# Performance work log

Measured on AMD Instinct MI355X. Metric: run time of the kernel, lower is better.

The kernel has to match this reference:

```python
import jax, jax.numpy as jnp
import numpy as np

NUM_GRAPHS = 64
BN_EPS = 1e-5


def setup_inputs() -> dict:
    key = jax.random.key(0)
    ks = jax.random.split(key, 20)
    N, E, D, H, C, L = 100_000, 1_600_000, 128, 128, 16, 4
    x = jax.random.normal(ks[0], (N, D), jnp.float32)
    edge_index = jax.random.randint(ks[1], (2, E), 0, N, jnp.int32)
    batch = jnp.sort(jax.random.randint(ks[2], (N,), 0, NUM_GRAPHS, jnp.int32))
    s = 0.05
    conv_W = jax.random.normal(ks[3], (L, D, H), jnp.float32) * s
    conv_b = jnp.zeros((L, H), jnp.float32)
    bn_gamma = jnp.ones((L, H), jnp.float32)
    bn_beta = jnp.zeros((L, H), jnp.float32)
    bn_mean = jax.random.normal(ks[4], (L, H), jnp.float32) * 0.01
    bn_var = jnp.ones((L, H), jnp.float32)
    cls_W1 = jax.random.normal(ks[5], (H, H), jnp.float32) * s
    cls_b1 = jnp.zeros((H,), jnp.float32)
    cls_W2 = jax.random.normal(ks[6], (H, C), jnp.float32) * s
    cls_b2 = jnp.zeros((C,), jnp.float32)
    nov_W1 = jax.random.normal(ks[7], (H, H), jnp.float32) * s
    nov_b1 = jnp.zeros((H,), jnp.float32)
    nov_W2 = jax.random.normal(ks[8], (H, 1), jnp.float32) * s
    nov_b2 = jnp.zeros((1,), jnp.float32)
    return {
        'x': x, 'edge_index': edge_index, 'batch': batch,
        'conv_W': conv_W, 'conv_b': conv_b,
        'bn_gamma': bn_gamma, 'bn_beta': bn_beta, 'bn_mean': bn_mean, 'bn_var': bn_var,
        'cls_W1': cls_W1, 'cls_b1': cls_b1, 'cls_W2': cls_W2, 'cls_b2': cls_b2,
        'nov_W1': nov_W1, 'nov_b1': nov_b1, 'nov_W2': nov_W2, 'nov_b2': nov_b2,
    }


def reference(x, edge_index, batch, conv_W, conv_b, bn_gamma, bn_beta, bn_mean, bn_var,
              cls_W1, cls_b1, cls_W2, cls_b2, nov_W1, nov_b1, nov_W2, nov_b2):
    N = x.shape[0]
    src, dst = edge_index[0], edge_index[1]
    # symmetric GCN normalization with self-loops: deg = in-degree + 1
    deg = jax.ops.segment_sum(jnp.ones(src.shape[0], x.dtype), dst, num_segments=N) + 1.0
    dis = jax.lax.rsqrt(deg)  # [N]
    edge_norm = (dis[src] * dis[dst])[:, None]  # [E,1]
    self_norm = (dis * dis)[:, None]            # [N,1]

    h = x
    for l in range(conv_W.shape[0]):
        hw = h @ conv_W[l]                                   # [N,H]
        agg = jax.ops.segment_sum(hw[src] * edge_norm, dst, num_segments=N)
        hw = agg + hw * self_norm + conv_b[l]                # GCNConv output
        # BatchNorm1d, eval mode (running stats); dropout is identity in eval
        hw = (hw - bn_mean[l]) * (bn_gamma[l] / jnp.sqrt(bn_var[l] + BN_EPS)) + bn_beta[l]
        h = jax.nn.relu(hw)

    pooled = jax.ops.segment_sum(h, batch, num_segments=NUM_GRAPHS)  # global_add_pool [G,H]
    logits = jax.nn.relu(pooled @ cls_W1 + cls_b1) @ cls_W2 + cls_b2           # [G,C]
    novelty = jax.nn.sigmoid(jax.nn.relu(pooled @ nov_W1 + nov_b1) @ nov_W2 + nov_b2)  # [G,1]
    return (logits, novelty)
```

## Files before the change

### kernel.cpp

```cpp
#include <hip/hip_runtime.h>
#include <hip/hip_fp16.h>
#include <cstdint>
#include <cstddef>

#define NUM_GRAPHS 64
#define HDIM 128
#define NBLK_S 256

typedef __attribute__((ext_vector_type(8))) _Float16 half8v;
typedef __attribute__((ext_vector_type(4))) float float4v;

__global__ __launch_bounds__(256) void count_hist_kernel(const int* __restrict__ dst,
                                                         int* __restrict__ cnt,
                                                         int* __restrict__ hist,
                                                         int E, int chunk, int shift, int NB) {
    __shared__ int lh[256];
    int t = threadIdx.x;
    int b = blockIdx.x;
    lh[t] = 0;
    __syncthreads();
    int beg = b * chunk;
    int end = beg + chunk; if (end > E) end = E;
    for (int i = beg + t; i < end; i += 256) {
        int d = dst[i];
        atomicAdd(&cnt[d], 1);
        atomicAdd(&lh[d >> shift], 1);
    }
    __syncthreads();
    for (int k = t; k < NB; k += 256) hist[k * NBLK_S + b] = lh[k];
}

__global__ __launch_bounds__(256) void scan_partial_kernel(const int* __restrict__ in,
                                                           int* __restrict__ blockSums, int M) {
    __shared__ int s[256];
    int t = threadIdx.x;
    int base = blockIdx.x * 4096 + t * 16;
    int local = 0;
#pragma unroll
    for (int i = 0; i < 16; ++i) {
        int idx = base + i;
        if (idx < M) local += in[idx];
    }
    s[t] = local;
    __syncthreads();
    for (int off = 128; off > 0; off >>= 1) {
        if (t < off) s[t] += s[t + off];
        __syncthreads();
    }
    if (t == 0) blockSums[blockIdx.x] = s[0];
}

__global__ __launch_bounds__(1024) void scan_blocksums_kernel(int* __restrict__ blockSums,
                                                              int* __restrict__ row_ptr_or_null,
                                                              int nb, int E, int N) {
    __shared__ int s[1024];
    int t = threadIdx.x;
    int v = (t < nb) ? blockSums[t] : 0;
    s[t] = v;
    __syncthreads();
    for (int off = 1; off < 1024; off <<= 1) {
        int u = (t >= off) ? s[t - off] : 0;
        __syncthreads();
        s[t] += u;
        __syncthreads();
    }
    if (t < nb) blockSums[t] = s[t] - v;
    if (t == 0 && row_ptr_or_null) row_ptr_or_null[N] = E;
}

__global__ __launch_bounds__(256) void scan_apply_kernel(const int* __restrict__ cnt,
                                                         const int* __restrict__ blockSums,
                                                         int* __restrict__ row_ptr,
                                                         int* __restrict__ fill,
                                                         float* __restrict__ dis, int N) {
    __shared__ int s[256];
    int t = threadIdx.x;
    int base = blockIdx.x * 4096 + t * 16;
    int c[16];
    int local = 0;
#pragma unroll
    for (int i = 0; i < 16; ++i) {
        int idx = base + i;
        c[i] = (idx < N) ? cnt[idx] : 0;
        local += c[i];
    }
    s[t] = local;
    __syncthreads();
    for (int off = 1; off < 256; off <<= 1) {
        int u = (t >= off) ? s[t - off] : 0;
        __syncthreads();
        s[t] += u;
        __syncthreads();
    }
    int pos = blockSums[blockIdx.x] + s[t] - local;
#pragma unroll
    for (int i = 0; i < 16; ++i) {
        int idx = base + i;
        if (idx < N) {
            row_ptr[idx] = pos;
            fill[idx] = pos;
            dis[idx] = rsqrtf((float)c[i] + 1.0f);
            pos += c[i];
        }
    }
}

__global__ __launch_bounds__(256) void scan_apply_generic(int* __restrict__ io,
                                                          const int* __restrict__ blockSums, int M) {
    __shared__ int s[256];
    int t = threadIdx.x;
    int base = blockIdx.x * 4096 + t * 16;
    int c[16];
    int local = 0;
#pragma unroll
    for (int i = 0; i < 16; ++i) {
        int idx = base + i;
        c[i] = (idx < M) ? io[idx] : 0;
        local += c[i];
    }
    s[t] = local;
    __syncthreads();
    for (int off = 1; off < 256; off <<= 1) {
        int u = (t >= off) ? s[t - off] : 0;
        __syncthreads();
        s[t] += u;
        __syncthreads();
    }
    int pos = blockSums[blockIdx.x] + s[t] - local;
#pragma unroll
    for (int i = 0; i < 16; ++i) {
        int idx = base + i;
        if (idx < M) {
            io[idx] = pos;
            pos += c[i];
        }
    }
}

__global__ __launch_bounds__(256) void scatter_bucket_kernel(const int* __restrict__ src,
                                                             const int* __restrict__ dst,
                                                             const int* __restrict__ hist,
                                                             int2* __restrict__ pairs,
                                                             int E, int chunk, int shift, int NB) {
    __shared__ int base[256];
    int t = threadIdx.x;
    int b = blockIdx.x;
    for (int k = t; k < NB; k += 256) base[k] = hist[k * NBLK_S + b];
    __syncthreads();
    int beg = b * chunk;
    int end = beg + chunk; if (end > E) end = E;
    for (int i = beg + t; i < end; i += 256) {
        int d = dst[i];
        int s = src[i];
        int pos = atomicAdd(&base[d >> shift], 1);
        pairs[pos] = make_int2(s, d);
    }
}

__global__ __launch_bounds__(256) void fill_pairs_kernel(const int2* __restrict__ pairs,
                                                         int* __restrict__ fill,
                                                         int* __restrict__ sorted_src, int E) {
    int i = blockIdx.x * 256 + threadIdx.x;
    if (i < E) {
        int2 p = pairs[i];
        int pos = atomicAdd(&fill[p.y], 1);
        sorted_src[pos] = p.x;
    }
}

__global__ __launch_bounds__(256) void fold_kernel(const float* __restrict__ gamma,
                                                   const float* __restrict__ beta,
                                                   const float* __restrict__ mean,
                                                   const float* __restrict__ var,
                                                   const float* __restrict__ convb,
                                                   float* __restrict__ scale,
                                                   float* __restrict__ bias, int LH) {
    int i = blockIdx.x * 256 + threadIdx.x;
    if (i < LH) {
        float gs = gamma[i] * rsqrtf(var[i] + 1e-5f);
        scale[i] = gs;
        bias[i] = (convb[i] - mean[i]) * gs + beta[i];
    }
}

__global__ __launch_bounds__(64) void pack_W_kernel(const float* __restrict__ W,
                                                    __half* __restrict__ hi,
                                                    __half* __restrict__ lo) {
    int b = blockIdx.x;
    int l = b >> 5;
    int ntile = (b >> 2) & 7;
    int kchunk = b & 3;
    int lane = threadIdx.x;
    int n = ntile * 16 + (lane & 15);
    int kbase = kchunk * 32 + (lane >> 4) * 8;
    size_t ob = ((size_t)b * 64 + lane) * 8;
#pragma unroll
    for (int j = 0; j < 8; ++j) {
        float w = W[(size_t)l * 16384 + (size_t)(kbase + j) * 128 + n];
        __half hb = __float2half_rn(w);
        float rem = w - __half2float(hb);
        hi[ob + j] = hb;
        lo[ob + j] = __float2half_rn(rem);
    }
}

__global__ __launch_bounds__(256) void gemm_mfma_f16(const __half* __restrict__ h16,
                                                     const float* __restrict__ h32,
                                                     const __half* __restrict__ Whi,
                                                     const __half* __restrict__ Wlo,
                                                     const float* __restrict__ dis,
                                                     __half* __restrict__ out, int N) {
    int wave = threadIdx.x >> 6;
    int lane = threadIdx.x & 63;
    int lrow = lane & 15;
    int lk8 = lane >> 4;
    int mbase = blockIdx.x * 128 + wave * 32;

    float4v acc[2][8];
#pragma unroll
    for (int mt = 0; mt < 2; ++mt)
#pragma unroll
        for (int nt = 0; nt < 8; ++nt) {
            acc[mt][nt][0] = 0.f; acc[mt][nt][1] = 0.f;
            acc[mt][nt][2] = 0.f; acc[mt][nt][3] = 0.f;
        }

    const half8v* BH = (const half8v*)Whi;
    const half8v* BL = (const half8v*)Wlo;
    const half8v* H8 = (const half8v*)h16;

    for (int kc = 0; kc < 4; ++kc) {
        half8v a[2];
#pragma unroll
        for (int mt = 0; mt < 2; ++mt) {
            int node = mbase + mt * 16 + lrow;
            if (node < N) {
                if (h32) {
                    const float4* hp = (const float4*)&h32[(size_t)node * HDIM + kc * 32 + lk8 * 8];
                    float4 f0 = hp[0], f1 = hp[1];
                    a[mt][0] = (_Float16)f0.x; a[mt][1] = (_Float16)f0.y;
                    a[mt][2] = (_Float16)f0.z; a[mt][3] = (_Float16)f0.w;
                    a[mt][4] = (_Float16)f1.x; a[mt][5] = (_Float16)f1.y;
                    a[mt][6] = (_Float16)f1.z; a[mt][7] = (_Float16)f1.w;
                } else {
                    a[mt] = H8[(size_t)node * 16 + kc * 4 + lk8];
                }
            } else {
#pragma unroll
                for (int j = 0; j < 8; ++j) a[mt][j] = (_Float16)0;
            }
        }
#pragma unroll
        for (int nt = 0; nt < 8; ++nt) {
            half8v bh = BH[(size_t)(nt * 4 + kc) * 64 + lane];
            half8v bl = BL[(size_t)(nt * 4 + kc) * 64 + lane];
#pragma unroll
            for (int mt = 0; mt < 2; ++mt) {
                acc[mt][nt] = __builtin_amdgcn_mfma_f32_16x16x32_f16(a[mt], bh, acc[mt][nt], 0, 0, 0);
                acc[mt][nt] = __builtin_amdgcn_mfma_f32_16x16x32_f16(a[mt], bl, acc[mt][nt], 0, 0, 0);
            }
        }
    }

#pragma unroll
    for (int mt = 0; mt < 2; ++mt) {
#pragma unroll
        for (int r = 0; r < 4; ++r) {
            int node = mbase + mt * 16 + lk8 * 4 + r;
            if (node < N) {
                float dn = dis[node];
#pragma unroll
                for (int nt = 0; nt < 8; ++nt)
                    out[(size_t)node * HDIM + nt * 16 + lrow] = __float2half_rn(acc[mt][nt][r] * dn);
            }
        }
    }
}

__device__ inline void acc_add8(float4& a, uint2 v) {
    float2 f0 = __half22float2(*(__half2*)&v.x);
    float2 f1 = __half22float2(*(__half2*)&v.y);
    a.x += f0.x; a.y += f0.y; a.z += f1.x; a.w += f1.y;
}

__global__ __launch_bounds__(256) void agg_kernel(const __half* __restrict__ hwp,
                                                  const int* __restrict__ row_ptr,
                                                  const int* __restrict__ ss,
                                                  const float* __restrict__ dis,
                                                  const float* __restrict__ scale,
                                                  const float* __restrict__ bias,
                                                  __half* __restrict__ hout, int N) {
    int wave = threadIdx.x >> 6;
    int lane = threadIdx.x & 63;
    int n = blockIdx.x * 4 + wave;
    if (n >= N) return;
    int hid = lane >> 5;
    int l32 = lane & 31;
    const uint2* rows = (const uint2*)hwp;

    float4 acc0 = make_float4(0.f, 0.f, 0.f, 0.f);
    float4 acc1 = make_float4(0.f, 0.f, 0.f, 0.f);

    if (hid == 0) {
        uint2 sv = rows[(size_t)n * 32 + l32];
        acc_add8(acc0, sv);
    }

    int e0 = row_ptr[n];
    int e1 = row_ptr[n + 1];
    int e = e0;

    for (; e + 15 < e1; e += 16) {
        int sA = ss[e + 0],  sB = ss[e + 1],  sC = ss[e + 2],  sD = ss[e + 3];
        int sE = ss[e + 4],  sF = ss[e + 5],  sG = ss[e + 6],  sH = ss[e + 7];
        int sI = ss[e + 8],  sJ = ss[e + 9],  sK = ss[e + 10], sL = ss[e + 11];
        int sM = ss[e + 12], sN = ss[e + 13], sO = ss[e + 14], sP = ss[e + 15];
        int q0 = hid ? sB : sA;
        int q1 = hid ? sD : sC;
        int q2 = hid ? sF : sE;
        int q3 = hid ? sH : sG;
        int q4 = hid ? sJ : sI;
        int q5 = hid ? sL : sK;
        int q6 = hid ? sN : sM;
        int q7 = hid ? sP : sO;
        uint2 v0 = rows[(size_t)q0 * 32 + l32];
        uint2 v1 = rows[(size_t)q1 * 32 + l32];
        uint2 v2 = rows[(size_t)q2 * 32 + l32];
        uint2 v3 = rows[(size_t)q3 * 32 + l32];
        uint2 v4 = rows[(size_t)q4 * 32 + l32];
        uint2 v5 = rows[(size_t)q5 * 32 + l32];
        uint2 v6 = rows[(size_t)q6 * 32 + l32];
        uint2 v7 = rows[(size_t)q7 * 32 + l32];
        acc_add8(acc0, v0);
        acc_add8(acc1, v1);
        acc_add8(acc0, v2);
        acc_add8(acc1, v3);
        acc_add8(acc0, v4);
        acc_add8(acc1, v5);
        acc_add8(acc0, v6);
        acc_add8(acc1, v7);
    }
    for (; e + 7 < e1; e += 8) {
        int sA = ss[e + 0], sB = ss[e + 1], sC = ss[e + 2], sD = ss[e + 3];
        int sE = ss[e + 4], sF = ss[e + 5], sG = ss[e + 6], sH = ss[e + 7];
        int q0 = hid ? sB : sA;
        int q1 = hid ? sD : sC;
        int q2 = hid ? sF : sE;
        int q3 = hid ? sH : sG;
        uint2 v0 = rows[(size_t)q0 * 32 + l32];
        uint2 v1 = rows[(size_t)q1 * 32 + l32];
        uint2 v2 = rows[(size_t)q2 * 32 + l32];
        uint2 v3 = rows[(size_t)q3 * 32 + l32];
        acc_add8(acc0, v0);
        acc_add8(acc1, v1);
        acc_add8(acc0, v2);
        acc_add8(acc1, v3);
    }
    for (; e + 1 < e1; e += 2) {
        int sA = ss[e], sB = ss[e + 1];
        int q0 = hid ? sB : sA;
        uint2 v0 = rows[(size_t)q0 * 32 + l32];
        acc_add8(acc0, v0);
    }
    if (e < e1) {
        if (hid == 0) {
            int sA = ss[e];
            uint2 v0 = rows[(size_t)sA * 32 + l32];
            acc_add8(acc1, v0);
        }
    }
    acc0.x += acc1.x; acc0.y += acc1.y; acc0.z += acc1.z; acc0.w += acc1.w;

    acc0.x += __shfl_xor(acc0.x, 32);
    acc0.y += __shfl_xor(acc0.y, 32);
    acc0.z += __shfl_xor(acc0.z, 32);
    acc0.w += __shfl_xor(acc0.w, 32);

    if (hid == 0) {
        float dn = dis[n];
        int f0 = l32 * 4;
        float4 sc = *(const float4*)&scale[f0];
        float4 bs = *(const float4*)&bias[f0];
        float y0 = fmaxf(dn * acc0.x * sc.x + bs.x, 0.f);
        float y1 = fmaxf(dn * acc0.y * sc.y + bs.y, 0.f);
        float y2 = fmaxf(dn * acc0.z * sc.z + bs.z, 0.f);
        float y3 = fmaxf(dn * acc0.w * sc.w + bs.w, 0.f);
        __half2 o0 = __floats2half2_rn(y0, y1);
        __half2 o1 = __floats2half2_rn(y2, y3);
        uint2 ov;
        ov.x = *(unsigned*)&o0;
        ov.y = *(unsigned*)&o1;
        ((uint2*)hout)[(size_t)n * 32 + l32] = ov;
    }
}

__global__ __launch_bounds__(256) void pool_kernel(const __half* __restrict__ h,
                                                   const int* __restrict__ batch,
                                                   float* __restrict__ pooled, int N) {
    int t = threadIdx.x;
    int grp = t >> 6;
    int lane = t & 63;
    int n0 = blockIdx.x * 64 + grp * 16;
    if (n0 >= N) return;
    int nend = n0 + 16; if (nend > N) nend = N;
    const __half2* h2 = (const __half2*)h;

    float2 acc = make_float2(0.f, 0.f);
    int cur = batch[n0];
    for (int n = n0; n < nend; ++n) {
        int gn = batch[n];
        if (gn != cur) {
            atomicAdd(&pooled[cur * HDIM + lane * 2], acc.x);
            atomicAdd(&pooled[cur * HDIM + lane * 2 + 1], acc.y);
            acc = make_float2(0.f, 0.f);
            cur = gn;
        }
        float2 v = __half22float2(h2[(size_t)n * 64 + lane]);
        acc.x += v.x;
        acc.y += v.y;
    }
    atomicAdd(&pooled[cur * HDIM + lane * 2], acc.x);
    atomicAdd(&pooled[cur * HDIM + lane * 2 + 1], acc.y);
}

__global__ __launch_bounds__(128) void head_kernel(const float* __restrict__ pooled,
                                                   const float* __restrict__ cW1, const float* __restrict__ cb1,
                                                   const float* __restrict__ cW2, const float* __restrict__ cb2,
                                                   const float* __restrict__ nW1, const float* __restrict__ nb1,
                                                   const float* __restrict__ nW2, const float* __restrict__ nb2,
                                                   float* __restrict__ out) {
    __shared__ float p[128];
    __shared__ float hid[128];
    int g = blockIdx.x, t = threadIdx.x;
    p[t] = pooled[g * HDIM + t];
    __syncthreads();

    float a = cb1[t];
    for (int k = 0; k < 128; ++k) a += p[k] * cW1[k * 128 + t];
    hid[t] = fmaxf(a, 0.f);
    __syncthreads();
    if (t < 16) {
        float acc = cb2[t];
        for (int j = 0; j < 128; ++j) acc += hid[j] * cW2[j * 16 + t];
        out[g * 16 + t] = acc;
    }
    __syncthreads();

    float b = nb1[t];
    for (int k = 0; k < 128; ++k) b += p[k] * nW1[k * 128 + t];
    hid[t] = fmaxf(b, 0.f);
    __syncthreads();
    if (t == 0) {
        float acc = nb2[0];
        for (int j = 0; j < 128; ++j) acc += hid[j] * nW2[j];
        out[NUM_GRAPHS * 16 + g] = 1.f / (1.f + expf(-acc));
    }
}

extern "C" void kernel_launch(void* const* d_in, const int* in_sizes, int n_in,
                              void* d_out, int out_size, void* d_ws, size_t ws_size,
                              hipStream_t stream) {
    const float* x       = (const float*)d_in[0];
    const int*   ei      = (const int*)d_in[1];
    const int*   batch   = (const int*)d_in[2];
    const float* conv_W  = (const float*)d_in[3];
    const float* conv_b  = (const float*)d_in[4];
    const float* bn_g    = (const float*)d_in[5];
    const float* bn_b    = (const float*)d_in[6];
    const float* bn_m    = (const float*)d_in[7];
    const float* bn_v    = (const float*)d_in[8];
    const float* cW1     = (const float*)d_in[9];
    const float* cb1     = (const float*)d_in[10];
    const float* cW2     = (const float*)d_in[11];
    const float* cb2     = (const float*)d_in[12];
    const float* nW1     = (const float*)d_in[13];
    const float* nb1     = (const float*)d_in[14];
    const float* nW2     = (const float*)d_in[15];
    const float* nb2     = (const float*)d_in[16];

    const int N = in_sizes[2];
    const int E = in_sizes[1] / 2;
    const int L = in_sizes[3] / (128 * 128);
    const int H = HDIM;

    const int* src = ei;
    const int* dst = ei + E;

    int shift = 9;
    while ((((N - 1) >> shift) + 1) > 256) ++shift;
    const int NB = ((N - 1) >> shift) + 1;
    const int M = NB * NBLK_S;
    const int chunk = (E + NBLK_S - 1) / NBLK_S;

    char* w = (char*)d_ws;
    size_t o = 0;
    auto alloc = [&](size_t bytes) -> void* {
        void* p = w + o;
        o = (o + bytes + 255) & ~(size_t)255;
        return p;
    };
    int nscanN = (N + 4095) / 4096;
    int nscanM = (M + 4095) / 4096;
    int nscanMax = nscanN > nscanM ? nscanN : nscanM;

    int*    cnt        = (int*)alloc((size_t)N * 4);
    int*    fill       = (int*)alloc((size_t)N * 4);
    int*    row_ptr    = (int*)alloc((size_t)(N + 1) * 4);
    float*  dis        = (float*)alloc((size_t)N * 4);
    float*  scale      = (float*)alloc((size_t)L * H * 4);
    float*  bias       = (float*)alloc((size_t)L * H * 4);
    int*    blockSums  = (int*)alloc((size_t)nscanMax * 4);
    int*    hist       = (int*)alloc((size_t)M * 4);
    int2*   pairs      = (int2*)alloc((size_t)E * 8);
    int*    sorted_src = (int*)alloc((size_t)E * 4);
    __half* Whi        = (__half*)alloc((size_t)L * H * H * 2);
    __half* Wlo        = (__half*)alloc((size_t)L * H * H * 2);
    __half* bufA       = (__half*)alloc((size_t)N * H * 2);
    __half* bufB       = (__half*)alloc((size_t)N * H * 2);
    float*  pooled     = (float*)alloc((size_t)NUM_GRAPHS * H * 4);

    hipMemsetAsync(cnt, 0, (size_t)N * 4, stream);
    hipMemsetAsync(pooled, 0, (size_t)NUM_GRAPHS * H * 4, stream);

    count_hist_kernel<<<NBLK_S, 256, 0, stream>>>(dst, cnt, hist, E, chunk, shift, NB);
    scan_partial_kernel<<<nscanN, 256, 0, stream>>>(cnt, blockSums, N);
    scan_blocksums_kernel<<<1, 1024, 0, stream>>>(blockSums, row_ptr, nscanN, E, N);
    scan_apply_kernel<<<nscanN, 256, 0, stream>>>(cnt, blockSums, row_ptr, fill, dis, N);
    scan_partial_kernel<<<nscanM, 256, 0, stream>>>(hist, blockSums, M);
    scan_blocksums_kernel<<<1, 1024, 0, stream>>>(blockSums, nullptr, nscanM, 0, 0);
    scan_apply_generic<<<nscanM, 256, 0, stream>>>(hist, blockSums, M);
    scatter_bucket_kernel<<<NBLK_S, 256, 0, stream>>>(src, dst, hist, pairs, E, chunk, shift, NB);
    fill_pairs_kernel<<<(E + 255) / 256, 256, 0, stream>>>(pairs, fill, sorted_src, E);

    fold_kernel<<<(L * H + 255) / 256, 256, 0, stream>>>(bn_g, bn_b, bn_m, bn_v, conv_b,
                                                         scale, bias, L * H);
    pack_W_kernel<<<L * 32, 64, 0, stream>>>(conv_W, Whi, Wlo);

    const __half* hin = nullptr;
    for (int l = 0; l < L; ++l) {
        gemm_mfma_f16<<<(N + 127) / 128, 256, 0, stream>>>(hin, l == 0 ? x : nullptr,
                                                           Whi + (size_t)l * H * H,
                                                           Wlo + (size_t)l * H * H,
                                                           dis, bufA, N);
        agg_kernel<<<(N + 3) / 4, 256, 0, stream>>>(bufA, row_ptr, sorted_src, dis,
                                                    scale + l * H, bias + l * H, bufB, N);
        hin = bufB;
    }

    pool_kernel<<<(N + 63) / 64, 256, 0, stream>>>(bufB, batch, pooled, N);
    head_kernel<<<NUM_GRAPHS, 128, 0, stream>>>(pooled, cW1, cb1, cW2, cb2,
                                                nW1, nb1, nW2, nb2, (float*)d_out);
}
```

Before: 695.8 us.

## Split GEMM output columns across waves and keep W fragments in registers

Reorganizes the per-layer feature GEMM so each wave owns two 16-column output tiles and holds its hi/lo weight fragments in registers for the whole block. The block now covers 64 rows instead of 128, with all four waves sharing the same rows, and the grid is doubled. This drops the 64 accumulators per wave and the repeated weight reloads. In exchange, every wave reloads the same A rows, so input reads per block grow about fourfold, mostly served from cache.

```diff
diff --git a/kernel.cpp b/kernel.cpp
--- a/kernel.cpp
+++ b/kernel.cpp
@@ -204,6 +204,30 @@
     }
 }
 
+__device__ inline half8v load_a(const half8v* __restrict__ H8,
+                                const float* __restrict__ h32,
+                                int node, int kc, int lk8, int N) {
+    half8v a;
+    if (node < N) {
+        if (h32) {
+            const float4* hp = (const float4*)&h32[(size_t)node * HDIM + kc * 32 + lk8 * 8];
+            float4 f0 = hp[0], f1 = hp[1];
+            a[0] = (_Float16)f0.x; a[1] = (_Float16)f0.y;
+            a[2] = (_Float16)f0.z; a[3] = (_Float16)f0.w;
+            a[4] = (_Float16)f1.x; a[5] = (_Float16)f1.y;
+            a[6] = (_Float16)f1.z; a[7] = (_Float16)f1.w;
+        } else {
+            a = H8[(size_t)node * 16 + kc * 4 + lk8];
+        }
+    } else {
+#pragma unroll
+        for (int j = 0; j < 8; ++j) a[j] = (_Float16)0;
+    }
+    return a;
+}
+
+#define MFMA16(A, B, C) __builtin_amdgcn_mfma_f32_16x16x32_f16((A), (B), (C), 0, 0, 0)
+
 __global__ __launch_bounds__(256) void gemm_mfma_f16(const __half* __restrict__ h16,
                                                      const float* __restrict__ h32,
                                                      const __half* __restrict__ Whi,
@@ -214,64 +238,59 @@
     int lane = threadIdx.x & 63;
     int lrow = lane & 15;
     int lk8 = lane >> 4;
-    int mbase = blockIdx.x * 128 + wave * 32;
-
-    float4v acc[2][8];
-#pragma unroll
-    for (int mt = 0; mt < 2; ++mt)
-#pragma unroll
-        for (int nt = 0; nt < 8; ++nt) {
-            acc[mt][nt][0] = 0.f; acc[mt][nt][1] = 0.f;
-            acc[mt][nt][2] = 0.f; acc[mt][nt][3] = 0.f;
-        }
+    int nt0 = wave * 2;
+    int mbase = blockIdx.x * 64;
+    if (mbase >= N) return;
 
     const half8v* BH = (const half8v*)Whi;
     const half8v* BL = (const half8v*)Wlo;
     const half8v* H8 = (const half8v*)h16;
 
-    for (int kc = 0; kc < 4; ++kc) {
-        half8v a[2];
-#pragma unroll
-        for (int mt = 0; mt < 2; ++mt) {
-            int node = mbase + mt * 16 + lrow;
-            if (node < N) {
-                if (h32) {
-                    const float4* hp = (const float4*)&h32[(size_t)node * HDIM + kc * 32 + lk8 * 8];
-                    float4 f0 = hp[0], f1 = hp[1];
-                    a[mt][0] = (_Float16)f0.x; a[mt][1] = (_Float16)f0.y;
-                    a[mt][2] = (_Float16)f0.z; a[mt][3] = (_Float16)f0.w;
-                    a[mt][4] = (_Float16)f1.x; a[mt][5] = (_Float16)f1.y;
-                    a[mt][6] = (_Float16)f1.z; a[mt][7] = (_Float16)f1.w;
-                } else {
-                    a[mt] = H8[(size_t)node * 16 + kc * 4 + lk8];
-                }
-            } else {
-#pragma unroll
-                for (int j = 0; j < 8; ++j) a[mt][j] = (_Float16)0;
-            }
-        }
-#pragma unroll
-        for (int nt = 0; nt < 8; ++nt) {
-            half8v bh = BH[(size_t)(nt * 4 + kc) * 64 + lane];
-            half8v bl = BL[(size_t)(nt * 4 + kc) * 64 + lane];
-#pragma unroll
-            for (int mt = 0; mt < 2; ++mt) {
-                acc[mt][nt] = __builtin_amdgcn_mfma_f32_16x16x32_f16(a[mt], bh, acc[mt][nt], 0, 0, 0);
-                acc[mt][nt] = __builtin_amdgcn_mfma_f32_16x16x32_f16(a[mt], bl, acc[mt][nt], 0, 0, 0);
-            }
-        }
-    }
-
-#pragma unroll
-    for (int mt = 0; mt < 2; ++mt) {
+    half8v bh00 = BH[(size_t)(nt0 * 4 + 0) * 64 + lane];
+    half8v bh01 = BH[(size_t)(nt0 * 4 + 1) * 64 + lane];
+    half8v bh02 = BH[(size_t)(nt0 * 4 + 2) * 64 + lane];
+    half8v bh03 = BH[(size_t)(nt0 * 4 + 3) * 64 + lane];
+    half8v bl00 = BL[(size_t)(nt0 * 4 + 0) * 64 + lane];
+    half8v bl01 = BL[(size_t)(nt0 * 4 + 1) * 64 + lane];
+    half8v bl02 = BL[(size_t)(nt0 * 4 + 2) * 64 + lane];
+    half8v bl03 = BL[(size_t)(nt0 * 4 + 3) * 64 + lane];
+    half8v bh10 = BH[(size_t)((nt0 + 1) * 4 + 0) * 64 + lane];
+    half8v bh11 = BH[(size_t)((nt0 + 1) * 4 + 1) * 64 + lane];
+    half8v bh12 = BH[(size_t)((nt0 + 1) * 4 + 2) * 64 + lane];
+    half8v bh13 = BH[(size_t)((nt0 + 1) * 4 + 3) * 64 + lane];
+    half8v bl10 = BL[(size_t)((nt0 + 1) * 4 + 0) * 64 + lane];
+    half8v bl11 = BL[(size_t)((nt0 + 1) * 4 + 1) * 64 + lane];
+    half8v bl12 = BL[(size_t)((nt0 + 1) * 4 + 2) * 64 + lane];
+    half8v bl13 = BL[(size_t)((nt0 + 1) * 4 + 3) * 64 + lane];
+
+#pragma unroll
+    for (int mt = 0; mt < 4; ++mt) {
+        int m0 = mbase + mt * 16;
+        if (m0 >= N) break;
+        int arow = m0 + lrow;
+        half8v a0 = load_a(H8, h32, arow, 0, lk8, N);
+        half8v a1 = load_a(H8, h32, arow, 1, lk8, N);
+        half8v a2 = load_a(H8, h32, arow, 2, lk8, N);
+        half8v a3 = load_a(H8, h32, arow, 3, lk8, N);
+
+        float4v c0 = {0.f, 0.f, 0.f, 0.f};
+        float4v c1 = {0.f, 0.f, 0.f, 0.f};
+        c0 = MFMA16(a0, bh00, c0); c0 = MFMA16(a0, bl00, c0);
+        c0 = MFMA16(a1, bh01, c0); c0 = MFMA16(a1, bl01, c0);
+        c0 = MFMA16(a2, bh02, c0); c0 = MFMA16(a2, bl02, c0);
+        c0 = MFMA16(a3, bh03, c0); c0 = MFMA16(a3, bl03, c0);
+        c1 = MFMA16(a0, bh10, c1); c1 = MFMA16(a0, bl10, c1);
+        c1 = MFMA16(a1, bh11, c1); c1 = MFMA16(a1, bl11, c1);
+        c1 = MFMA16(a2, bh12, c1); c1 = MFMA16(a2, bl12, c1);
+        c1 = MFMA16(a3, bh13, c1); c1 = MFMA16(a3, bl13, c1);
+
 #pragma unroll
         for (int r = 0; r < 4; ++r) {
-            int node = mbase + mt * 16 + lk8 * 4 + r;
+            int node = m0 + lk8 * 4 + r;
             if (node < N) {
                 float dn = dis[node];
-#pragma unroll
-                for (int nt = 0; nt < 8; ++nt)
-                    out[(size_t)node * HDIM + nt * 16 + lrow] = __float2half_rn(acc[mt][nt][r] * dn);
+                out[(size_t)node * HDIM + nt0 * 16 + lrow] = __float2half_rn(c0[r] * dn);
+                out[(size_t)node * HDIM + nt0 * 16 + 16 + lrow] = __float2half_rn(c1[r] * dn);
             }
         }
     }
@@ -538,10 +557,10 @@
 
     const __half* hin = nullptr;
     for (int l = 0; l < L; ++l) {
-        gemm_mfma_f16<<<(N + 127) / 128, 256, 0, stream>>>(hin, l == 0 ? x : nullptr,
-                                                           Whi + (size_t)l * H * H,
-                                                           Wlo + (size_t)l * H * H,
-                                                           dis, bufA, N);
+        gemm_mfma_f16<<<(N + 63) / 64, 256, 0, stream>>>(hin, l == 0 ? x : nullptr,
+                                                         Whi + (size_t)l * H * H,
+                                                         Wlo + (size_t)l * H * H,
+                                                         dis, bufA, N);
         agg_kernel<<<(N + 3) / 4, 256, 0, stream>>>(bufA, row_ptr, sorted_src, dis,
                                                     scale + l * H, bias + l * H, bufB, N);
         hin = bufB;
```

Result: no change. 700.3 us (+0.6%).
